# Optimization experiments

Hardware: AMD Instinct MI355X
Metric: run time of the kernel (lower is better)

Reference implementation:

```python
import jax, jax.numpy as jnp
import numpy as np


def setup_inputs() -> dict:
    key = jax.random.key(0)
    k1, k2, k3, k4 = jax.random.split(key, 4)
    B, N, C, H, W = 32, 25, 512, 14, 14
    DK, DV = 128, 128
    return {
        "query_repr": jax.random.normal(k1, (B, C, H, W), dtype=jnp.float32),
        "supports_repr": jax.random.normal(k2, (B, N, C, H, W), dtype=jnp.float32),
        "W_qk": jax.random.normal(k3, (DK, C), dtype=jnp.float32) * (C ** -0.5),
        "W_v": jax.random.normal(k4, (DV, C), dtype=jnp.float32) * (C ** -0.5),
    }


def reference(query_repr, supports_repr, W_qk, W_v):
    # 1x1 convs == channel contractions
    b, c, h, w = query_repr.shape
    n = supports_repr.shape[1]
    query_q = jnp.einsum('kc,bchw->bkhw', W_qk, query_repr)      # [b, dk, h, w]
    query_v = jnp.einsum('vc,bchw->bvhw', W_v, query_repr)       # [b, dv, h, w]
    supports_k = jnp.einsum('kc,bncij->bnkij', W_qk, supports_repr)
    supports_v = jnpp = jnp.einsum('vc,bncij->bnvij', W_v, supports_repr)

    # cross-attention: each query spatial position attends over all support
    # images and their spatial positions jointly
    sim = jnp.einsum('bchw,bncij->bhwnij', query_q, supports_k)  # [b,h,w,n,i,j]
    sim_flat = sim.reshape(b, h, w, n * h * w)
    attn = jax.nn.softmax(sim_flat, axis=-1).reshape(b, h, w, n, h, w)
    out = jnp.einsum('bhwnij,bncij->bchw', attn, supports_v)     # [b, dv, h, w]

    euclidean_dist = jnp.sum((query_v - out) ** 2) / (h * w)
    return euclidean_dist
```

## Files before the change

kernel.cpp:

```cpp
#include <hip/hip_runtime.h>

#define NB   32
#define NSUP 25
#define NC   512
#define NHW  196
#define NDK  128
#define NPT  4900
#define NPTP 4928

typedef short  bf16x8 __attribute__((ext_vector_type(8)));
typedef float  f32x4  __attribute__((ext_vector_type(4)));
typedef float  f32x4v __attribute__((ext_vector_type(4)));
typedef unsigned short ushort;
typedef unsigned int   uint;
typedef ushort ushort4v __attribute__((ext_vector_type(4)));
typedef uint   uint2v   __attribute__((ext_vector_type(2)));

static __device__ __forceinline__ ushort f2bf(float f) {
    union { float f; uint u; } v; v.f = f;
    uint r = v.u + 0x7fffu + ((v.u >> 16) & 1u);
    return (ushort)(r >> 16);
}

static __device__ __forceinline__ f32x4 mfma16(bf16x8 a, bf16x8 b, f32x4 c) {
    return __builtin_amdgcn_mfma_f32_16x16x32_bf16(a, b, c, 0, 0, 0);
}

__global__ __launch_bounds__(256) void k_cast(
    const float* __restrict__ Wqk, const float* __restrict__ Wv,
    ushort* __restrict__ Wc)
{
    int i = blockIdx.x * 256 + threadIdx.x;
    const float* src = (i < 16384) ? Wqk : Wv;
    int j = (i < 16384) ? i : i - 16384;
    f32x4 v = *(const f32x4*)(src + (size_t)j * 4);
    ushort4v u;
    u[0] = f2bf(v[0]); u[1] = f2bf(v[1]); u[2] = f2bf(v[2]); u[3] = f2bf(v[3]);
    *(ushort4v*)(Wc + (size_t)i * 4) = u;
}

__global__ __launch_bounds__(256) void k_zpad(ushort* __restrict__ sv)
{
    int i = blockIdx.x * 256 + threadIdx.x;
    if (i < 4096 * 14) {
        int row = i / 14, j = i - row * 14;
        ((uint*)sv)[(size_t)row * (NPTP / 2) + (NPT / 2) + j] = 0u;
    }
}

template<int PBASE, int NT, int PG>
__global__ __launch_bounds__(512) void k_proj(
    const float* __restrict__ query, const float* __restrict__ supports,
    const ushort* __restrict__ Wc,
    ushort* __restrict__ sk, ushort* __restrict__ sv,
    ushort* __restrict__ qq, float* __restrict__ qv)
{
    __shared__ __align__(16) ushort Xl[112 * 64];
    const int n = blockIdx.x;
    const int b = blockIdx.y;
    const float* X = (n < NSUP)
        ? (supports + (size_t)(b * NSUP + n) * NC * NHW)
        : (query + (size_t)b * NC * NHW);
    const int t = threadIdx.x;
    const int w = t >> 6, l = t & 63;
    const int m0 = w * 32;
    const int l15 = l & 15, l4 = l >> 4;

    f32x4 acc[2][NT];
#pragma unroll
    for (int mi = 0; mi < 2; ++mi)
#pragma unroll
        for (int nt = 0; nt < NT; ++nt) acc[mi][nt] = (f32x4){0.f, 0.f, 0.f, 0.f};

    for (int kt = 0; kt < NC; kt += 64) {
        if (kt) __syncthreads();
        for (int pass = 0; pass < 2; ++pass) {
            int idx = t + pass * 512;
            if (idx < 32 * PG) {
                int kp = idx / PG;
                int pg = idx - kp * PG;
                const float* r0 = X + (size_t)(kt + 2 * kp) * NHW + PBASE + pg * 4;
                f32x4 f0 = *(const f32x4*)r0;
                f32x4 f1 = *(const f32x4*)(r0 + NHW);
                int cq = kp >> 2;
#pragma unroll
                for (int j = 0; j < 4; ++j) {
                    int p = pg * 4 + j;
                    uint wd = (uint)f2bf(f0[j]) | ((uint)f2bf(f1[j]) << 16);
                    ((uint*)Xl)[p * 32 + ((cq ^ (p & 7)) << 2) + (kp & 3)] = wd;
                }
            }
        }
        __syncthreads();
#pragma unroll
        for (int kkh = 0; kkh < 2; ++kkh) {
            const ushort* wrow = Wc + (size_t)(m0 + l15) * NC + kt + kkh * 32 + l4 * 8;
            bf16x8 a0 = *(const bf16x8*)wrow;
            bf16x8 a1 = *(const bf16x8*)(wrow + 16 * NC);
#pragma unroll
            for (int nt = 0; nt < NT; ++nt) {
                int p = nt * 16 + l15;
                int cq = kkh * 4 + l4;
                bf16x8 bf = *(const bf16x8*)&Xl[p * 64 + ((cq ^ (p & 7)) << 3)];
                acc[0][nt] = mfma16(a0, bf, acc[0][nt]);
                acc[1][nt] = mfma16(a1, bf, acc[1][nt]);
            }
        }
    }

#pragma unroll
    for (int nt = 0; nt < NT; ++nt) {
        int p = PBASE + nt * 16 + l15;
        if (p >= NHW) continue;
#pragma unroll
        for (int mi = 0; mi < 2; ++mi) {
            int dbase = m0 + mi * 16 + l4 * 4;
            f32x4 v = acc[mi][nt];
            if (n < NSUP) {
                int pgl = n * NHW + p;
                if (dbase < NDK) {
                    ushort4v u;
                    u[0] = f2bf(v[0]); u[1] = f2bf(v[1]);
                    u[2] = f2bf(v[2]); u[3] = f2bf(v[3]);
                    *(ushort4v*)&sk[((size_t)b * NPT + pgl) * NDK + dbase] = u;
                } else {
                    int dv = dbase - NDK;
#pragma unroll
                    for (int r = 0; r < 4; ++r)
                        sv[((size_t)b * NDK + dv + r) * NPTP + pgl] = f2bf(v[r]);
                }
            } else {
                if (dbase < NDK) {
                    ushort4v u;
                    u[0] = f2bf(v[0]); u[1] = f2bf(v[1]);
                    u[2] = f2bf(v[2]); u[3] = f2bf(v[3]);
                    *(ushort4v*)&qq[((size_t)b * NHW + p) * NDK + dbase] = u;
                } else {
                    *(f32x4*)&qv[((size_t)b * NHW + p) * NDK + (dbase - NDK)] = v;
                }
            }
        }
    }
}

__global__ __launch_bounds__(256) void k_sim(
    const ushort* __restrict__ qq, const ushort* __restrict__ sk,
    float* __restrict__ sim)
{
    const int b = blockIdx.y;
    const int t = threadIdx.x, l = t & 63;
    const int l15 = l & 15, l4 = l >> 4;
    const int pw = blockIdx.x * 64 + (t >> 6) * 16;

    int pA = pw + l15; if (pA > NPT - 1) pA = NPT - 1;
    const ushort* Ab = sk + ((size_t)b * NPT + pA) * NDK + l4 * 8;
    const ushort* Bb = qq + (size_t)b * NHW * NDK + l4 * 8;

    f32x4 acc[13];
#pragma unroll
    for (int st = 0; st < 13; ++st) acc[st] = (f32x4){0.f, 0.f, 0.f, 0.f};

#pragma unroll
    for (int k0 = 0; k0 < 128; k0 += 32) {
        bf16x8 a = *(const bf16x8*)(Ab + k0);
#pragma unroll
        for (int st = 0; st < 13; ++st) {
            int s = st * 16 + l15; if (s > NHW - 1) s = NHW - 1;
            bf16x8 bf = *(const bf16x8*)(Bb + (size_t)s * NDK + k0);
            acc[st] = mfma16(a, bf, acc[st]);
        }
    }

    int pst = pw + l4 * 4;
#pragma unroll
    for (int st = 0; st < 13; ++st) {
        int s = st * 16 + l15;
        if (s < NHW && pst + 3 < NPT)
            *(f32x4*)&sim[((size_t)b * NHW + s) * NPT + pst] = acc[st];
    }
}

__global__ __launch_bounds__(256) void k_attn(
    const float* __restrict__ sim, const ushort* __restrict__ sv,
    const float* __restrict__ qv, float* __restrict__ out)
{
    __shared__ __align__(16) ushort Pl[16 * 72];
    __shared__ float rsP[16 * 16];
    __shared__ float rsum[16];
    __shared__ float wred[4];
    const int b = blockIdx.y;
    const int s0 = blockIdx.x * 16;
    const int t = threadIdx.x;
    const int w = t >> 6, l = t & 63;
    const int l15 = l & 15, l4 = l >> 4;
    const int sl = t >> 4;
    const int pq = (t & 15) * 4;
    const int sg = s0 + sl;
    const bool srow_ok = (sg < NHW);
    const float* simrow = sim + ((size_t)b * NHW + (srow_ok ? sg : 0)) * NPT;
    const ushort* svb = sv + (size_t)b * NDK * NPTP;

    float psum = 0.f;
    f32x4 acc[2];
    acc[0] = (f32x4){0.f, 0.f, 0.f, 0.f};
    acc[1] = (f32x4){0.f, 0.f, 0.f, 0.f};

    for (int ch = 0; ch < 77; ++ch) {
        const int p0 = ch * 64;
        __syncthreads();
        float e0 = 0.f, e1 = 0.f, e2 = 0.f, e3 = 0.f;
        if (srow_ok && (p0 + pq) < NPT) {
            f32x4 xv = *(const f32x4*)(simrow + p0 + pq);
            e0 = __expf(xv[0] - 60.f);
            e1 = __expf(xv[1] - 60.f);
            e2 = __expf(xv[2] - 60.f);
            e3 = __expf(xv[3] - 60.f);
            psum += e0 + e1 + e2 + e3;
        }
        uint2v wd;
        wd[0] = (uint)f2bf(e0) | ((uint)f2bf(e1) << 16);
        wd[1] = (uint)f2bf(e2) | ((uint)f2bf(e3) << 16);
        *(uint2v*)&Pl[sl * 72 + pq] = wd;
        __syncthreads();
        bf16x8 a0 = *(const bf16x8*)&Pl[l15 * 72 + l4 * 8];
        bf16x8 a1 = *(const bf16x8*)&Pl[l15 * 72 + 32 + l4 * 8];
#pragma unroll
        for (int nt = 0; nt < 2; ++nt) {
            int d = w * 32 + nt * 16 + l15;
            const ushort* svd = svb + (size_t)d * NPTP + p0 + l4 * 8;
            bf16x8 b0 = *(const bf16x8*)svd;
            bf16x8 b1 = *(const bf16x8*)(svd + 32);
            acc[nt] = mfma16(a0, b0, acc[nt]);
            acc[nt] = mfma16(a1, b1, acc[nt]);
        }
    }

    rsP[sl * 16 + (t & 15)] = psum;
    __syncthreads();
    if (t < 16) {
        float s = 0.f;
#pragma unroll
        for (int j = 0; j < 16; ++j) s += rsP[t * 16 + j];
        rsum[t] = s;
    }
    __syncthreads();

    float part = 0.f;
#pragma unroll
    for (int nt = 0; nt < 2; ++nt) {
        int d = w * 32 + nt * 16 + l15;
#pragma unroll
        for (int r = 0; r < 4; ++r) {
            int sr = l4 * 4 + r;
            int s = s0 + sr;
            if (s < NHW) {
                float o = acc[nt][r] / rsum[sr];
                float q = qv[((size_t)b * NHW + s) * NDK + d];
                float df = q - o;
                part = fmaf(df, df, part);
            }
        }
    }
#pragma unroll
    for (int off = 32; off > 0; off >>= 1) part += __shfl_down(part, off, 64);
    if (l == 0) wred[w] = part;
    __syncthreads();
    if (t == 0)
        atomicAdd(out, (wred[0] + wred[1] + wred[2] + wred[3]) * (1.0f / 196.0f));
}

extern "C" void kernel_launch(void* const* d_in, const int* in_sizes, int n_in,
                              void* d_out, int out_size, void* d_ws, size_t ws_size,
                              hipStream_t stream)
{
    const float* query    = (const float*)d_in[0];
    const float* supports = (const float*)d_in[1];
    const float* Wqk      = (const float*)d_in[2];
    const float* Wv       = (const float*)d_in[3];
    float* out = (float*)d_out;

    char* ws = (char*)d_ws;
    ushort* Wc  = (ushort*)ws;                         ws += (size_t)256 * NC * 2;
    ushort* sk  = (ushort*)ws;                         ws += (size_t)NB * NPT * NDK * 2;
    ushort* sv  = (ushort*)ws;                         ws += (size_t)NB * NDK * NPTP * 2;
    ushort* qq  = (ushort*)ws;                         ws += (size_t)NB * NHW * NDK * 2;
    float*  qv  = (float*)ws;                          ws += (size_t)NB * NHW * NDK * 4;
    float*  sim = (float*)ws;

    hipMemsetAsync(d_out, 0, (size_t)out_size * sizeof(float), stream);
    k_cast<<<128, 256, 0, stream>>>(Wqk, Wv, Wc);
    k_zpad<<<224, 256, 0, stream>>>(sv);
    k_proj<0,   7, 28><<<dim3(NSUP + 1, NB), 512, 0, stream>>>(query, supports, Wc, sk, sv, qq, qv);
    k_proj<112, 6, 21><<<dim3(NSUP + 1, NB), 512, 0, stream>>>(query, supports, Wc, sk, sv, qq, qv);
    k_sim<<<dim3(77, NB), 256, 0, stream>>>(qq, sk, sim);
    k_attn<<<dim3(13, NB), 256, 0, stream>>>(sim, sv, qv, out);
}
```

Measured before the change: 765.1 us.

## Fuse similarity GEMM into attention kernel and merge projection into one pass

The similarity scores are now computed inside the attention kernel with MFMA, chunk by chunk, instead of being written to a large fp32 sim buffer and read back. This removes a full round trip of that buffer through global memory. The two half-image projection launches become one kernel that stages its outputs through LDS to get coalesced sk, sv and qq stores. The attention grid is remapped so the batches are spread across XCDs. The zero-padding kernel for sv is dropped, so the padded tail of sv may now be left uninitialized when it is multiplied by zero probabilities.

```diff
diff --git a/kernel.cpp b/kernel.cpp
--- a/kernel.cpp
+++ b/kernel.cpp
@@ -10,18 +10,15 @@
 
 typedef short  bf16x8 __attribute__((ext_vector_type(8)));
 typedef float  f32x4  __attribute__((ext_vector_type(4)));
-typedef float  f32x4v __attribute__((ext_vector_type(4)));
 typedef unsigned short ushort;
 typedef unsigned int   uint;
 typedef ushort ushort4v __attribute__((ext_vector_type(4)));
-typedef uint   uint2v   __attribute__((ext_vector_type(2)));
 
 static __device__ __forceinline__ ushort f2bf(float f) {
     union { float f; uint u; } v; v.f = f;
     uint r = v.u + 0x7fffu + ((v.u >> 16) & 1u);
     return (ushort)(r >> 16);
 }
-
 static __device__ __forceinline__ f32x4 mfma16(bf16x8 a, bf16x8 b, f32x4 c) {
     return __builtin_amdgcn_mfma_f32_16x16x32_bf16(a, b, c, 0, 0, 0);
 }
@@ -39,223 +36,246 @@
     *(ushort4v*)(Wc + (size_t)i * 4) = u;
 }
 
-__global__ __launch_bounds__(256) void k_zpad(ushort* __restrict__ sv)
-{
-    int i = blockIdx.x * 256 + threadIdx.x;
-    if (i < 4096 * 14) {
-        int row = i / 14, j = i - row * 14;
-        ((uint*)sv)[(size_t)row * (NPTP / 2) + (NPT / 2) + j] = 0u;
-    }
-}
-
-template<int PBASE, int NT, int PG>
 __global__ __launch_bounds__(512) void k_proj(
     const float* __restrict__ query, const float* __restrict__ supports,
     const ushort* __restrict__ Wc,
     ushort* __restrict__ sk, ushort* __restrict__ sv,
     ushort* __restrict__ qq, float* __restrict__ qv)
 {
-    __shared__ __align__(16) ushort Xl[112 * 64];
-    const int n = blockIdx.x;
-    const int b = blockIdx.y;
-    const float* X = (n < NSUP)
-        ? (supports + (size_t)(b * NSUP + n) * NC * NHW)
-        : (query + (size_t)b * NC * NHW);
+    __shared__ __align__(16) ushort Sb[15360];
+    const int n = blockIdx.x, b = blockIdx.y;
+    const bool isq = (n == NSUP);
+    const float* X = isq ? (query + (size_t)b * NC * NHW)
+                         : (supports + (size_t)(b * NSUP + n) * NC * NHW);
     const int t = threadIdx.x;
-    const int w = t >> 6, l = t & 63;
-    const int m0 = w * 32;
-    const int l15 = l & 15, l4 = l >> 4;
-
-    f32x4 acc[2][NT];
-#pragma unroll
-    for (int mi = 0; mi < 2; ++mi)
-#pragma unroll
-        for (int nt = 0; nt < NT; ++nt) acc[mi][nt] = (f32x4){0.f, 0.f, 0.f, 0.f};
+    const int w = t >> 6, l = t & 63, l15 = l & 15, l4 = l >> 4;
+    const int dB = w >> 1;
+    const int pg = w & 1;
+    const int NTw = 7 - pg;
+
+    f32x4 acc[4][7];
+#pragma unroll
+    for (int mi = 0; mi < 4; ++mi)
+#pragma unroll
+        for (int nt = 0; nt < 7; ++nt) acc[mi][nt] = (f32x4){0.f, 0.f, 0.f, 0.f};
 
     for (int kt = 0; kt < NC; kt += 64) {
         if (kt) __syncthreads();
-        for (int pass = 0; pass < 2; ++pass) {
-            int idx = t + pass * 512;
-            if (idx < 32 * PG) {
-                int kp = idx / PG;
-                int pg = idx - kp * PG;
-                const float* r0 = X + (size_t)(kt + 2 * kp) * NHW + PBASE + pg * 4;
-                f32x4 f0 = *(const f32x4*)r0;
-                f32x4 f1 = *(const f32x4*)(r0 + NHW);
-                int cq = kp >> 2;
-#pragma unroll
-                for (int j = 0; j < 4; ++j) {
-                    int p = pg * 4 + j;
-                    uint wd = (uint)f2bf(f0[j]) | ((uint)f2bf(f1[j]) << 16);
-                    ((uint*)Xl)[p * 32 + ((cq ^ (p & 7)) << 2) + (kp & 3)] = wd;
+#pragma unroll
+        for (int pass = 0; pass < 7; ++pass) {
+            int idx = pass * 512 + t;
+            if (idx < 3136) {
+                int kq = idx & 3, rest = idx >> 2;
+                int pp = rest % 98, kb = rest / 98;
+                int kp = kb * 4 + kq;
+                const float* src = X + (size_t)(kt + 2 * kp) * NHW + 2 * pp;
+                float2 f0 = *(const float2*)src;
+                float2 f1 = *(const float2*)(src + NHW);
+#pragma unroll
+                for (int j = 0; j < 2; ++j) {
+                    int p = 2 * pp + j;
+                    float a0 = j ? f0.y : f0.x;
+                    float a1 = j ? f1.y : f1.x;
+                    uint wd = (uint)f2bf(a0) | ((uint)f2bf(a1) << 16);
+                    uint off = (uint)(p * 128 + kp * 4) ^ ((uint)(p & 7) << 4);
+                    *(uint*)((char*)Sb + off) = wd;
                 }
             }
         }
         __syncthreads();
 #pragma unroll
         for (int kkh = 0; kkh < 2; ++kkh) {
-            const ushort* wrow = Wc + (size_t)(m0 + l15) * NC + kt + kkh * 32 + l4 * 8;
-            bf16x8 a0 = *(const bf16x8*)wrow;
-            bf16x8 a1 = *(const bf16x8*)(wrow + 16 * NC);
-#pragma unroll
-            for (int nt = 0; nt < NT; ++nt) {
-                int p = nt * 16 + l15;
-                int cq = kkh * 4 + l4;
-                bf16x8 bf = *(const bf16x8*)&Xl[p * 64 + ((cq ^ (p & 7)) << 3)];
-                acc[0][nt] = mfma16(a0, bf, acc[0][nt]);
-                acc[1][nt] = mfma16(a1, bf, acc[1][nt]);
+            bf16x8 bw[4];
+#pragma unroll
+            for (int mi = 0; mi < 4; ++mi)
+                bw[mi] = *(const bf16x8*)&Wc[(size_t)(dB * 64 + mi * 16 + l15) * NC
+                                             + kt + kkh * 32 + l4 * 8];
+#pragma unroll
+            for (int nt = 0; nt < 7; ++nt) {
+                if (nt < NTw) {
+                    int p = (pg * 7 + nt) * 16 + l15;
+                    uint off = (uint)(p * 128 + kkh * 64 + l4 * 16)
+                               ^ ((uint)(p & 7) << 4);
+                    bf16x8 ax = *(const bf16x8*)((char*)Sb + off);
+#pragma unroll
+                    for (int mi = 0; mi < 4; ++mi)
+                        acc[mi][nt] = mfma16(ax, bw[mi], acc[mi][nt]);
+                }
             }
         }
     }
 
-#pragma unroll
-    for (int nt = 0; nt < NT; ++nt) {
-        int p = PBASE + nt * 16 + l15;
-        if (p >= NHW) continue;
-#pragma unroll
-        for (int mi = 0; mi < 2; ++mi) {
-            int dbase = m0 + mi * 16 + l4 * 4;
-            f32x4 v = acc[mi][nt];
-            if (n < NSUP) {
-                int pgl = n * NHW + p;
-                if (dbase < NDK) {
-                    ushort4v u;
-                    u[0] = f2bf(v[0]); u[1] = f2bf(v[1]);
-                    u[2] = f2bf(v[2]); u[3] = f2bf(v[3]);
-                    *(ushort4v*)&sk[((size_t)b * NPT + pgl) * NDK + dbase] = u;
+#pragma unroll 1
+    for (int part = 0; part < 2; ++part) {
+#pragma unroll 1
+        for (int ph = 0; ph < 2; ++ph) {
+            __syncthreads();
+            const bool mywave = (pg == ph) && ((dB >> 1) == part);
+            if (mywave) {
+                const int dloc = (dB & 1) * 64;
+                if (part == 0) {
+#pragma unroll
+                    for (int mi = 0; mi < 4; ++mi)
+#pragma unroll
+                        for (int nt = 0; nt < 7; ++nt) {
+                            if (nt < NTw) {
+                                int d = dloc + mi * 16 + l15;
+#pragma unroll
+                                for (int r = 0; r < 4; ++r) {
+                                    int p = nt * 16 + l4 * 4 + r;
+                                    uint off = (uint)((p * 136 + d) * 2)
+                                               ^ ((uint)(p & 7) << 4);
+                                    *(ushort*)((char*)Sb + off) = f2bf(acc[mi][nt][r]);
+                                }
+                            }
+                        }
+                } else if (!isq) {
+#pragma unroll
+                    for (int mi = 0; mi < 4; ++mi)
+#pragma unroll
+                        for (int nt = 0; nt < 7; ++nt) {
+                            if (nt < NTw) {
+                                int d = dloc + mi * 16 + l15;
+                                int p = nt * 16 + l4 * 4;
+                                ushort4v u;
+#pragma unroll
+                                for (int r = 0; r < 4; ++r) u[r] = f2bf(acc[mi][nt][r]);
+                                uint off = (uint)((d * 120 + p) * 2)
+                                           ^ ((uint)(d & 7) << 4);
+                                *(ushort4v*)((char*)Sb + off) = u;
+                            }
+                        }
                 } else {
-                    int dv = dbase - NDK;
-#pragma unroll
-                    for (int r = 0; r < 4; ++r)
-                        sv[((size_t)b * NDK + dv + r) * NPTP + pgl] = f2bf(v[r]);
-                }
-            } else {
-                if (dbase < NDK) {
-                    ushort4v u;
-                    u[0] = f2bf(v[0]); u[1] = f2bf(v[1]);
-                    u[2] = f2bf(v[2]); u[3] = f2bf(v[3]);
-                    *(ushort4v*)&qq[((size_t)b * NHW + p) * NDK + dbase] = u;
-                } else {
-                    *(f32x4*)&qv[((size_t)b * NHW + p) * NDK + (dbase - NDK)] = v;
+#pragma unroll
+                    for (int mi = 0; mi < 4; ++mi)
+#pragma unroll
+                        for (int nt = 0; nt < 7; ++nt) {
+                            if (nt < NTw) {
+                                int d = dloc + mi * 16 + l15;
+#pragma unroll
+                                for (int r = 0; r < 4; ++r) {
+                                    int p = (pg * 7 + nt) * 16 + l4 * 4 + r;
+                                    if (p < NHW)
+                                        qv[((size_t)b * NHW + p) * NDK + d] = acc[mi][nt][r];
+                                }
+                            }
+                        }
+                }
+            }
+            __syncthreads();
+            if (part == 0) {
+                for (int idx = t; idx < 112 * 16; idx += 512) {
+                    int row = idx >> 4, c = idx & 15;
+                    int pimg = ph * 112 + row;
+                    if (pimg < NHW) {
+                        uint off = (uint)(row * 272 + c * 16) ^ ((uint)(row & 7) << 4);
+                        bf16x8 vv = *(const bf16x8*)((char*)Sb + off);
+                        ushort* dst = isq
+                            ? &qq[((size_t)b * NHW + pimg) * NDK + c * 8]
+                            : &sk[((size_t)b * NPT + n * NHW + pimg) * NDK + c * 8];
+                        *(bf16x8*)dst = vv;
+                    }
+                }
+            } else if (!isq) {
+                int nch = (ph == 0) ? 14 : 11;
+                for (int idx = t; idx < 128 * nch; idx += 512) {
+                    int d = idx / nch, c = idx - d * nch;
+                    int pl = c * 8;
+                    int pimg = ph * 112 + pl;
+                    uint off = (uint)((d * 120 + pl) * 2) ^ ((uint)(d & 7) << 4);
+                    ushort* dst = &sv[((size_t)b * NDK + d) * NPTP
+                                      + (size_t)n * NHW + pimg];
+                    if (pimg + 7 < NHW) {
+                        ushort4v v0 = *(const ushort4v*)((char*)Sb + off);
+                        ushort4v v1 = *(const ushort4v*)((char*)Sb + off + 8);
+                        *(ushort4v*)dst = v0;
+                        *(ushort4v*)(dst + 4) = v1;
+                    } else if (pimg < NHW) {
+                        ushort4v v0 = *(const ushort4v*)((char*)Sb + off);
+                        *(ushort4v*)dst = v0;
+                    }
                 }
             }
         }
     }
 }
 
-__global__ __launch_bounds__(256) void k_sim(
+__global__ __launch_bounds__(256) void k_attn(
     const ushort* __restrict__ qq, const ushort* __restrict__ sk,
-    float* __restrict__ sim)
+    const ushort* __restrict__ sv, const float* __restrict__ qv,
+    float* __restrict__ out)
 {
-    const int b = blockIdx.y;
-    const int t = threadIdx.x, l = t & 63;
-    const int l15 = l & 15, l4 = l >> 4;
-    const int pw = blockIdx.x * 64 + (t >> 6) * 16;
-
-    int pA = pw + l15; if (pA > NPT - 1) pA = NPT - 1;
-    const ushort* Ab = sk + ((size_t)b * NPT + pA) * NDK + l4 * 8;
-    const ushort* Bb = qq + (size_t)b * NHW * NDK + l4 * 8;
-
-    f32x4 acc[13];
-#pragma unroll
-    for (int st = 0; st < 13; ++st) acc[st] = (f32x4){0.f, 0.f, 0.f, 0.f};
-
-#pragma unroll
-    for (int k0 = 0; k0 < 128; k0 += 32) {
-        bf16x8 a = *(const bf16x8*)(Ab + k0);
-#pragma unroll
-        for (int st = 0; st < 13; ++st) {
-            int s = st * 16 + l15; if (s > NHW - 1) s = NHW - 1;
-            bf16x8 bf = *(const bf16x8*)(Bb + (size_t)s * NDK + k0);
-            acc[st] = mfma16(a, bf, acc[st]);
-        }
-    }
-
-    int pst = pw + l4 * 4;
-#pragma unroll
-    for (int st = 0; st < 13; ++st) {
-        int s = st * 16 + l15;
-        if (s < NHW && pst + 3 < NPT)
-            *(f32x4*)&sim[((size_t)b * NHW + s) * NPT + pst] = acc[st];
-    }
-}
-
-__global__ __launch_bounds__(256) void k_attn(
-    const float* __restrict__ sim, const ushort* __restrict__ sv,
-    const float* __restrict__ qv, float* __restrict__ out)
-{
-    __shared__ __align__(16) ushort Pl[16 * 72];
-    __shared__ float rsP[16 * 16];
-    __shared__ float rsum[16];
+    __shared__ __align__(16) ushort Pl[16 * 80];
+    __shared__ float rsP[4][16];
+    __shared__ float rinv[16];
     __shared__ float wred[4];
-    const int b = blockIdx.y;
-    const int s0 = blockIdx.x * 16;
+    const int bid = blockIdx.x;
+    const int xcd = bid & 7, slot = bid >> 3;
+    const int b = xcd + 8 * (slot & 3);
+    const int st = slot >> 2;
+    const int s0 = st * 16;
     const int t = threadIdx.x;
-    const int w = t >> 6, l = t & 63;
-    const int l15 = l & 15, l4 = l >> 4;
-    const int sl = t >> 4;
-    const int pq = (t & 15) * 4;
-    const int sg = s0 + sl;
-    const bool srow_ok = (sg < NHW);
-    const float* simrow = sim + ((size_t)b * NHW + (srow_ok ? sg : 0)) * NPT;
-    const ushort* svb = sv + (size_t)b * NDK * NPTP;
-
+    const int w = t >> 6, l = t & 63, l15 = l & 15, l4 = l >> 4;
+
+    const int sq = min(s0 + l15, NHW - 1);
+    bf16x8 qf[4];
+#pragma unroll
+    for (int ks = 0; ks < 4; ++ks)
+        qf[ks] = *(const bf16x8*)&qq[((size_t)b * NHW + sq) * NDK + ks * 32 + l4 * 8];
+
+    f32x4 oacc[2];
+    oacc[0] = (f32x4){0.f, 0.f, 0.f, 0.f};
+    oacc[1] = (f32x4){0.f, 0.f, 0.f, 0.f};
     float psum = 0.f;
-    f32x4 acc[2];
-    acc[0] = (f32x4){0.f, 0.f, 0.f, 0.f};
-    acc[1] = (f32x4){0.f, 0.f, 0.f, 0.f};
 
     for (int ch = 0; ch < 77; ++ch) {
         const int p0 = ch * 64;
+        const int pa = min(p0 + w * 16 + l15, NPT - 1);
+        const ushort* arow = &sk[((size_t)b * NPT + pa) * NDK + l4 * 8];
+        f32x4 sacc = (f32x4){0.f, 0.f, 0.f, 0.f};
+#pragma unroll
+        for (int ks = 0; ks < 4; ++ks)
+            sacc = mfma16(*(const bf16x8*)(arow + ks * 32), qf[ks], sacc);
+        ushort4v u;
+#pragma unroll
+        for (int r = 0; r < 4; ++r) {
+            int p = p0 + w * 16 + l4 * 4 + r;
+            float e = (p < NPT) ? __expf(sacc[r] - 60.f) : 0.f;
+            psum += e;
+            u[r] = f2bf(e);
+        }
+        *(ushort4v*)&Pl[l15 * 80 + w * 16 + l4 * 4] = u;
         __syncthreads();
-        float e0 = 0.f, e1 = 0.f, e2 = 0.f, e3 = 0.f;
-        if (srow_ok && (p0 + pq) < NPT) {
-            f32x4 xv = *(const f32x4*)(simrow + p0 + pq);
-            e0 = __expf(xv[0] - 60.f);
-            e1 = __expf(xv[1] - 60.f);
-            e2 = __expf(xv[2] - 60.f);
-            e3 = __expf(xv[3] - 60.f);
-            psum += e0 + e1 + e2 + e3;
-        }
-        uint2v wd;
-        wd[0] = (uint)f2bf(e0) | ((uint)f2bf(e1) << 16);
-        wd[1] = (uint)f2bf(e2) | ((uint)f2bf(e3) << 16);
-        *(uint2v*)&Pl[sl * 72 + pq] = wd;
+        bf16x8 a0 = *(const bf16x8*)&Pl[l15 * 80 + l4 * 8];
+        bf16x8 a1 = *(const bf16x8*)&Pl[l15 * 80 + 32 + l4 * 8];
+#pragma unroll
+        for (int dt = 0; dt < 2; ++dt) {
+            int d = w * 32 + dt * 16 + l15;
+            const ushort* svd = &sv[((size_t)b * NDK + d) * NPTP + p0 + l4 * 8];
+            oacc[dt] = mfma16(a0, *(const bf16x8*)svd, oacc[dt]);
+            oacc[dt] = mfma16(a1, *(const bf16x8*)(svd + 32), oacc[dt]);
+        }
         __syncthreads();
-        bf16x8 a0 = *(const bf16x8*)&Pl[l15 * 72 + l4 * 8];
-        bf16x8 a1 = *(const bf16x8*)&Pl[l15 * 72 + 32 + l4 * 8];
-#pragma unroll
-        for (int nt = 0; nt < 2; ++nt) {
-            int d = w * 32 + nt * 16 + l15;
-            const ushort* svd = svb + (size_t)d * NPTP + p0 + l4 * 8;
-            bf16x8 b0 = *(const bf16x8*)svd;
-            bf16x8 b1 = *(const bf16x8*)(svd + 32);
-            acc[nt] = mfma16(a0, b0, acc[nt]);
-            acc[nt] = mfma16(a1, b1, acc[nt]);
-        }
     }
 
-    rsP[sl * 16 + (t & 15)] = psum;
+    psum += __shfl_down(psum, 32, 64);
+    psum += __shfl_down(psum, 16, 64);
+    if (l < 16) rsP[w][l] = psum;
     __syncthreads();
-    if (t < 16) {
-        float s = 0.f;
-#pragma unroll
-        for (int j = 0; j < 16; ++j) s += rsP[t * 16 + j];
-        rsum[t] = s;
-    }
+    if (t < 16) rinv[t] = 1.0f / (rsP[0][t] + rsP[1][t] + rsP[2][t] + rsP[3][t]);
     __syncthreads();
 
     float part = 0.f;
 #pragma unroll
-    for (int nt = 0; nt < 2; ++nt) {
-        int d = w * 32 + nt * 16 + l15;
+    for (int dt = 0; dt < 2; ++dt) {
+        int d = w * 32 + dt * 16 + l15;
 #pragma unroll
         for (int r = 0; r < 4; ++r) {
-            int sr = l4 * 4 + r;
-            int s = s0 + sr;
-            if (s < NHW) {
-                float o = acc[nt][r] / rsum[sr];
-                float q = qv[((size_t)b * NHW + s) * NDK + d];
+            int s = l4 * 4 + r;
+            int sg = s0 + s;
+            if (sg < NHW) {
+                float o = oacc[dt][r] * rinv[s];
+                float q = qv[((size_t)b * NHW + sg) * NDK + d];
                 float df = q - o;
                 part = fmaf(df, df, part);
             }
@@ -280,18 +300,15 @@
     float* out = (float*)d_out;
 
     char* ws = (char*)d_ws;
-    ushort* Wc  = (ushort*)ws;                         ws += (size_t)256 * NC * 2;
-    ushort* sk  = (ushort*)ws;                         ws += (size_t)NB * NPT * NDK * 2;
-    ushort* sv  = (ushort*)ws;                         ws += (size_t)NB * NDK * NPTP * 2;
-    ushort* qq  = (ushort*)ws;                         ws += (size_t)NB * NHW * NDK * 2;
-    float*  qv  = (float*)ws;                          ws += (size_t)NB * NHW * NDK * 4;
-    float*  sim = (float*)ws;
+    ushort* Wc = (ushort*)ws;  ws += (size_t)256 * NC * 2;
+    ushort* sk = (ushort*)ws;  ws += (size_t)NB * NPT * NDK * 2;
+    ushort* sv = (ushort*)ws;  ws += (size_t)NB * NDK * NPTP * 2;
+    ushort* qq = (ushort*)ws;  ws += (size_t)NB * NHW * NDK * 2;
+    float*  qv = (float*)ws;
 
     hipMemsetAsync(d_out, 0, (size_t)out_size * sizeof(float), stream);
     k_cast<<<128, 256, 0, stream>>>(Wqk, Wv, Wc);
-    k_zpad<<<224, 256, 0, stream>>>(sv);
-    k_proj<0,   7, 28><<<dim3(NSUP + 1, NB), 512, 0, stream>>>(query, supports, Wc, sk, sv, qq, qv);
-    k_proj<112, 6, 21><<<dim3(NSUP + 1, NB), 512, 0, stream>>>(query, supports, Wc, sk, sv, qq, qv);
-    k_sim<<<dim3(77, NB), 256, 0, stream>>>(qq, sk, sim);
-    k_attn<<<dim3(13, NB), 256, 0, stream>>>(sim, sv, qv, out);
-}
+    k_proj<<<dim3(NSUP + 1, NB), 512, 0, stream>>>(query, supports, Wc,
+                                                   sk, sv, qq, qv);
+    k_attn<<<416, 256, 0, stream>>>(qq, sk, sv, qv, out);
+}
```

New measurement: 1.059 ms. 38.4% more time.
